# Optimization experiments

Hardware: AMD Instinct MI355X
Metric: run time of the kernel (lower is better)

The kernel has to match this reference:

```python
import jax, jax.numpy as jnp
import numpy as np
from jax import ops

NEG_SLOPE = 0.2
EPS = 1e-5


def layer_norm(v, g, b):
    mu = jnp.mean(v, axis=-1, keepdims=True)
    var = jnp.mean(jnp.square(v - mu), axis=-1, keepdims=True)
    return (v - mu) * jax.lax.rsqrt(var + EPS) * g + b


def gat_conv(x, src, dst, W, a_src, a_dst, bias, N, H, C, concat):
    # linear projection, per-head view [N, H, C]
    h = (x @ W).reshape(N, H, C)
    alpha_src = jnp.sum(h * a_src, axis=-1)  # [N, H]
    alpha_dst = jnp.sum(h * a_dst, axis=-1)  # [N, H]
    # per-edge raw attention logits [E, H]
    e = alpha_src[src] + alpha_dst[dst]
    e = jnp.where(e > 0, e, NEG_SLOPE * e)  # leaky relu
    # segment softmax over destination node
    m = ops.segment_max(e, dst, num_segments=N)  # [N, H]
    a = jnp.exp(e - m[dst])
    s = ops.segment_sum(a, dst, num_segments=N)  # [N, H]
    a = a / s[dst]
    # weighted scatter-aggregate: [E, H, C] messages -> [N, H, C]
    out = ops.segment_sum(h[src] * a[:, :, None], dst, num_segments=N)
    if concat:
        return out.reshape(N, H * C) + bias
    return jnp.mean(out, axis=1) + bias


def setup_inputs() -> dict:
    key = jax.random.key(0)
    ks = jax.random.split(key, 16)
    N, E, IN, H, C1, C2 = 50000, 800000, 128, 4, 64, 64
    sd_in = 1.0 / np.sqrt(IN)
    sd_h = 1.0 / np.sqrt(H * C1)
    return {
        "x": jax.random.normal(ks[0], (N, IN), jnp.float32),
        "edge_index": jax.random.randint(ks[1], (2, E), 0, N, jnp.int64),
        # GAT layer 1 (in -> H*C1, concat)
        "W1": jax.random.normal(ks[2], (IN, H * C1), jnp.float32) * sd_in,
        "att_src1": jax.random.normal(ks[3], (H, C1), jnp.float32) * sd_in,
        "att_dst1": jax.random.normal(ks[4], (H, C1), jnp.float32) * sd_in,
        "bias1": jnp.zeros((H * C1,), jnp.float32),
        "g1": jnp.ones((H * C1,), jnp.float32),
        "b1": jnp.zeros((H * C1,), jnp.float32),
        # GAT layer 2 (H*C1 -> C2, mean over heads)
        "W2": jax.random.normal(ks[5], (H * C1, H * C2), jnp.float32) * sd_h,
        "att_src2": jax.random.normal(ks[6], (H, C2), jnp.float32) * sd_h,
        "att_dst2": jax.random.normal(ks[7], (H, C2), jnp.float32) * sd_h,
        "bias2": jnp.zeros((C2,), jnp.float32),
        "g2": jnp.ones((C2,), jnp.float32),
        "b2": jnp.zeros((C2,), jnp.float32),
        # residual projection (in != out)
        "Wres": jax.random.normal(ks[8], (IN, C2), jnp.float32) * sd_in,
        "bres": jnp.zeros((C2,), jnp.float32),
    }


def reference(x, edge_index, W1, att_src1, att_dst1, bias1, g1, b1,
              W2, att_src2, att_dst2, bias2, g2, b2, Wres, bres):
    N = x.shape[0]
    H, C1 = att_src1.shape
    C2 = att_src2.shape[1]
    # PyG GATConv add_self_loops=True
    loop = jnp.arange(N, dtype=edge_index.dtype)
    src = jnp.concatenate([edge_index[0], loop])
    dst = jnp.concatenate([edge_index[1], loop])

    identity = x @ Wres + bres
    h1 = gat_conv(x, src, dst, W1, att_src1, att_dst1, bias1, N, H, C1, concat=True)
    h1 = jax.nn.elu(layer_norm(h1, g1, b1))  # dropout inactive (eval)
    h2 = gat_conv(h1, src, dst, W2, att_src2, att_dst2, bias2, N, H, C2, concat=False)
    h2 = layer_norm(h2, g2, b2)
    return jax.nn.elu(h2 + identity)
```

## Files before the change

### kernel.cpp

```cpp
#include <hip/hip_runtime.h>
#include <math.h>

#define HH 4
#define CC 64
#define HC 256
#define CAP 96

static constexpr float NEG_SLOPE = 0.2f;
static constexpr float LN_EPS = 1e-5f;

typedef __attribute__((ext_vector_type(8))) short short8;
typedef __attribute__((ext_vector_type(4))) float floatx4;
typedef __attribute__((ext_vector_type(4))) unsigned int uintx4;

__device__ __forceinline__ float bf2f(unsigned short u) {
  return __uint_as_float(((unsigned int)u) << 16);
}
__device__ __forceinline__ unsigned short f2bf(float f) {
  unsigned int u = __float_as_uint(f);
  u = (u + 0x7fff + ((u >> 16) & 1)) >> 16;
  return (unsigned short)u;
}
__device__ __forceinline__ unsigned int pack2bf(float a, float b) {
  return (unsigned int)f2bf(a) | ((unsigned int)f2bf(b) << 16);
}

__device__ __forceinline__ void macc8(float* acc, uintx4 h, float w) {
  acc[0] += w * __uint_as_float(h.x << 16);
  acc[1] += w * __uint_as_float(h.x & 0xffff0000u);
  acc[2] += w * __uint_as_float(h.y << 16);
  acc[3] += w * __uint_as_float(h.y & 0xffff0000u);
  acc[4] += w * __uint_as_float(h.z << 16);
  acc[5] += w * __uint_as_float(h.z & 0xffff0000u);
  acc[6] += w * __uint_as_float(h.w << 16);
  acc[7] += w * __uint_as_float(h.w & 0xffff0000u);
}

__device__ __forceinline__ short8 ldA8(const unsigned short* A, size_t idx) {
  return *(const short8*)(A + idx);
}
__device__ __forceinline__ short8 ldA8(const float* A, size_t idx) {
  const float4 u = *(const float4*)(A + idx);
  const float4 v = *(const float4*)(A + idx + 4);
  short8 r;
  r[0] = (short)f2bf(u.x); r[1] = (short)f2bf(u.y);
  r[2] = (short)f2bf(u.z); r[3] = (short)f2bf(u.w);
  r[4] = (short)f2bf(v.x); r[5] = (short)f2bf(v.y);
  r[6] = (short)f2bf(v.z); r[7] = (short)f2bf(v.w);
  return r;
}

__global__ __launch_bounds__(256) void prep_kernel(
    const float* __restrict__ W1, const float* __restrict__ W2,
    const float* __restrict__ Wres,
    unsigned short* __restrict__ wt1c, unsigned short* __restrict__ wt2,
    int* __restrict__ deg, int N) {
  const int idx = blockIdx.x * 256 + threadIdx.x;
  if (idx < 49152) {
    const int r = idx >> 7, k = idx & 127;
    float v = 0.f;
    if (r < 256) v = W1[k * 256 + r];
    else if (r < 320) v = Wres[k * 64 + (r - 256)];
    wt1c[idx] = f2bf(v);
  } else if (idx < 49152 + 65536) {
    const int i = idx - 49152;
    const int r = i >> 8, k = i & 255;
    wt2[i] = f2bf(W2[k * 256 + r]);
  } else if (idx < 49152 + 65536 + N) {
    deg[idx - 49152 - 65536] = 0;
  }
}

__global__ __launch_bounds__(256) void scatter_bump(
    const int* __restrict__ srcs, const int* __restrict__ dsts,
    int* __restrict__ deg, int* __restrict__ col, int E, int N) {
  const int e = blockIdx.x * 256 + threadIdx.x;
  if (e >= E + N) return;
  int s, d;
  if (e < E) { s = srcs[e]; d = dsts[e]; }
  else       { s = e - E; d = s; }
  const int pos = atomicAdd(&deg[d], 1);
  col[d * CAP + pos] = s;
}

template <typename AT>
__global__ __launch_bounds__(256) void gemm128(
    const AT* __restrict__ A, const unsigned short* __restrict__ BT,
    unsigned short* __restrict__ Chm,
    float* __restrict__ ident, const float* __restrict__ bres,
    const float* __restrict__ att_src, const float* __restrict__ att_dst,
    float* __restrict__ as_, float* __restrict__ ad_,
    int M, int K) {
  __shared__ unsigned short As[128][40];
  __shared__ unsigned short Bs[128][40];
  const int tid = threadIdx.x;
  const int w = tid >> 6, lane = tid & 63;
  const int q = lane >> 4, mr = lane & 15;
  const int rh = w >> 1, ch = w & 1;
  const int row0 = blockIdx.x * 128;
  const int col0 = blockIdx.y * 128;
  const int sr = tid >> 2;
  const int sk = (tid & 3) * 8;

  floatx4 acc[4][4] = {};

  short8 a0 = {}, a1 = {}, b0, b1;
  {
    const int r0 = row0 + sr, r1 = row0 + sr + 64;
    if (r0 < M) a0 = ldA8(A, (size_t)r0 * K + sk);
    if (r1 < M) a1 = ldA8(A, (size_t)r1 * K + sk);
    b0 = *(const short8*)(BT + (size_t)(col0 + sr) * K + sk);
    b1 = *(const short8*)(BT + (size_t)(col0 + sr + 64) * K + sk);
  }
  for (int k0 = 0; k0 < K; k0 += 32) {
    *(short8*)(&As[sr][sk]) = a0;
    *(short8*)(&As[sr + 64][sk]) = a1;
    *(short8*)(&Bs[sr][sk]) = b0;
    *(short8*)(&Bs[sr + 64][sk]) = b1;
    __syncthreads();
    const int kn = k0 + 32;
    if (kn < K) {
      const int r0 = row0 + sr, r1 = row0 + sr + 64;
      a0 = (r0 < M) ? ldA8(A, (size_t)r0 * K + kn + sk) : short8{};
      a1 = (r1 < M) ? ldA8(A, (size_t)r1 * K + kn + sk) : short8{};
      b0 = *(const short8*)(BT + (size_t)(col0 + sr) * K + kn + sk);
      b1 = *(const short8*)(BT + (size_t)(col0 + sr + 64) * K + kn + sk);
    }
    short8 af[4], bf[4];
#pragma unroll
    for (int i = 0; i < 4; ++i)
      af[i] = *(const short8*)(&As[rh * 64 + i * 16 + mr][q * 8]);
#pragma unroll
    for (int j = 0; j < 4; ++j)
      bf[j] = *(const short8*)(&Bs[ch * 64 + j * 16 + mr][q * 8]);
#pragma unroll
    for (int i = 0; i < 4; ++i)
#pragma unroll
      for (int j = 0; j < 4; ++j)
        acc[i][j] = __builtin_amdgcn_mfma_f32_16x16x32_bf16(af[i], bf[j], acc[i][j], 0, 0, 0);
    __syncthreads();
  }
  if (col0 < 256) {
    const int hh = (col0 >> 6) + ch;
#pragma unroll
    for (int i = 0; i < 4; ++i)
#pragma unroll
      for (int j = 0; j < 4; ++j)
#pragma unroll
        for (int rr = 0; rr < 4; ++rr) {
          const int row = row0 + rh * 64 + i * 16 + q * 4 + rr;
          if (row < M)
            Chm[((size_t)hh * M + row) * 64 + j * 16 + mr] = f2bf(acc[i][j][rr]);
        }
    float pa[16] = {}, pb[16] = {};
#pragma unroll
    for (int j = 0; j < 4; ++j) {
      const float a_s = att_src[hh * 64 + j * 16 + mr];
      const float a_d = att_dst[hh * 64 + j * 16 + mr];
#pragma unroll
      for (int i = 0; i < 4; ++i)
#pragma unroll
        for (int rr = 0; rr < 4; ++rr) {
          pa[i * 4 + rr] += acc[i][j][rr] * a_s;
          pb[i * 4 + rr] += acc[i][j][rr] * a_d;
        }
    }
#pragma unroll
    for (int off = 1; off < 16; off <<= 1) {
#pragma unroll
      for (int t = 0; t < 16; ++t) {
        pa[t] += __shfl_xor(pa[t], off);
        pb[t] += __shfl_xor(pb[t], off);
      }
    }
    if (mr == 0) {
#pragma unroll
      for (int i = 0; i < 4; ++i)
#pragma unroll
        for (int rr = 0; rr < 4; ++rr) {
          const int row = row0 + rh * 64 + i * 16 + q * 4 + rr;
          if (row < M) {
            as_[row * 4 + hh] = pa[i * 4 + rr];
            ad_[row * 4 + hh] = pb[i * 4 + rr];
          }
        }
    }
  } else if (ch == 0) {
#pragma unroll
    for (int i = 0; i < 4; ++i)
#pragma unroll
      for (int j = 0; j < 4; ++j)
#pragma unroll
        for (int rr = 0; rr < 4; ++rr) {
          const int row = row0 + rh * 64 + i * 16 + q * 4 + rr;
          if (row < M) {
            const int cc = j * 16 + mr;
            ident[(size_t)row * 64 + cc] = acc[i][j][rr] + bres[cc];
          }
        }
  }
}

__global__ __launch_bounds__(256) void agg_gather(
    const int* __restrict__ deg, const int* __restrict__ col,
    const float* __restrict__ as_, const float* __restrict__ ad_,
    const unsigned short* __restrict__ hlin_hm,
    unsigned short* __restrict__ agg, int N) {
  const int b = blockIdx.x;
  const int hh = b & 3;
  const int w = threadIdx.x >> 6, lane = threadIdx.x & 63;
  const int g = lane >> 4;
  const int sub = (lane >> 3) & 1;
  const int cg = lane & 7;
  const int el = lane & 15;
  const int gb = lane & 48;
  const int n = (b >> 3) * 32 + ((b >> 2) & 1) * 16 + w * 4 + g;
  const bool valid = n < N;
  const int n_c = valid ? n : 0;
  const uintx4* hb = (const uintx4*)(hlin_hm + (size_t)hh * N * 64) + cg;
  const float adv = ad_[n_c * 4 + hh];
  const int cnt = valid ? deg[n_c] : 0;
  const int* cbase = col + n_c * CAP;
  float acc[8] = {};
  float wsum = 0.f;
  for (int off = 0;; off += 16) {
    const int len = cnt - off;
    int lm = len > 16 ? 16 : (len < 0 ? 0 : len);
    lm = max(lm, __shfl_xor(lm, 16));
    lm = max(lm, __shfl_xor(lm, 32));
    if (lm == 0) break;
    int s_l = 0;
    float w_l = 0.f;
    if (el < len) {
      s_l = cbase[off + el];
      float v = as_[s_l * 4 + hh] + adv;
      v = v > 0.f ? v : NEG_SLOPE * v;
      w_l = __expf(v);
    }
    wsum += w_l;
    int j = 0;
    for (; j + 4 <= lm; j += 4) {
      const int sA = __shfl(s_l, gb + j + sub);
      const int sB = __shfl(s_l, gb + j + 2 + sub);
      const float wA = __shfl(w_l, gb + j + sub);
      const float wB = __shfl(w_l, gb + j + 2 + sub);
      const uintx4 hA = hb[(size_t)sA * 8];
      const uintx4 hB = hb[(size_t)sB * 8];
      macc8(acc, hA, wA);
      macc8(acc, hB, wB);
    }
    for (; j < lm; j += 2) {
      const int s = __shfl(s_l, gb + j + sub);
      const float wt = __shfl(w_l, gb + j + sub);
      macc8(acc, hb[(size_t)s * 8], wt);
    }
  }
  wsum += __shfl_xor(wsum, 1);
  wsum += __shfl_xor(wsum, 2);
  wsum += __shfl_xor(wsum, 4);
  wsum += __shfl_xor(wsum, 8);
#pragma unroll
  for (int t = 0; t < 8; ++t) acc[t] += __shfl_xor(acc[t], 8);
  if (sub == 0 && valid) {
    const float inv = 1.0f / wsum;
    uintx4 o;
    o.x = pack2bf(acc[0] * inv, acc[1] * inv);
    o.y = pack2bf(acc[2] * inv, acc[3] * inv);
    o.z = pack2bf(acc[4] * inv, acc[5] * inv);
    o.w = pack2bf(acc[6] * inv, acc[7] * inv);
    ((uintx4*)(agg + ((size_t)hh * N + n) * 64))[cg] = o;
  }
}

__global__ __launch_bounds__(256) void combine_ln1(
    const unsigned short* __restrict__ agg, const float* __restrict__ bias1,
    const float* __restrict__ g1, const float* __restrict__ b1,
    unsigned short* __restrict__ h1, int N) {
  const int n = blockIdx.x;
  const int tid = threadIdx.x;
  const int hh = tid >> 6, lane = tid & 63;
  const float val = bf2f(agg[((size_t)hh * N + n) * 64 + lane]) + bias1[tid];
  float s1 = val, s2 = val * val;
#pragma unroll
  for (int off = 32; off > 0; off >>= 1) {
    s1 += __shfl_down(s1, off);
    s2 += __shfl_down(s2, off);
  }
  __shared__ float ws1[4], ws2[4];
  if (lane == 0) { ws1[hh] = s1; ws2[hh] = s2; }
  __syncthreads();
  const float tot1 = ws1[0] + ws1[1] + ws1[2] + ws1[3];
  const float tot2 = ws2[0] + ws2[1] + ws2[2] + ws2[3];
  const float mu = tot1 * (1.0f / HC);
  const float var = tot2 * (1.0f / HC) - mu * mu;
  float y = (val - mu) * rsqrtf(var + LN_EPS) * g1[tid] + b1[tid];
  y = y > 0.f ? y : expm1f(y);
  h1[(size_t)n * HC + tid] = f2bf(y);
}

__global__ __launch_bounds__(256) void combine_final(
    const unsigned short* __restrict__ agg, const float* __restrict__ ident,
    const float* __restrict__ bias2, const float* __restrict__ g2,
    const float* __restrict__ b2, float* __restrict__ out, int N) {
  const int n = blockIdx.x * 4 + (threadIdx.x >> 6);
  const int c = threadIdx.x & 63;
  if (n >= N) return;
  float v = 0.25f * (bf2f(agg[((size_t)0 * N + n) * 64 + c]) +
                     bf2f(agg[((size_t)1 * N + n) * 64 + c]) +
                     bf2f(agg[((size_t)2 * N + n) * 64 + c]) +
                     bf2f(agg[((size_t)3 * N + n) * 64 + c])) +
            bias2[c];
  float s1 = v, s2 = v * v;
#pragma unroll
  for (int off = 32; off > 0; off >>= 1) {
    s1 += __shfl_down(s1, off);
    s2 += __shfl_down(s2, off);
  }
  s1 = __shfl(s1, 0);
  s2 = __shfl(s2, 0);
  const float mu = s1 * (1.0f / 64.0f);
  const float var = s2 * (1.0f / 64.0f) - mu * mu;
  float y = (v - mu) * rsqrtf(var + LN_EPS) * g2[c] + b2[c];
  y += ident[(size_t)n * 64 + c];
  out[(size_t)n * 64 + c] = y > 0.f ? y : expm1f(y);
}

extern "C" void kernel_launch(void* const* d_in, const int* in_sizes, int n_in,
                              void* d_out, int out_size, void* d_ws, size_t ws_size,
                              hipStream_t stream) {
  const float* x        = (const float*)d_in[0];
  const int*   ei       = (const int*)d_in[1];
  const float* W1       = (const float*)d_in[2];
  const float* att_src1 = (const float*)d_in[3];
  const float* att_dst1 = (const float*)d_in[4];
  const float* bias1    = (const float*)d_in[5];
  const float* g1       = (const float*)d_in[6];
  const float* b1       = (const float*)d_in[7];
  const float* W2       = (const float*)d_in[8];
  const float* att_src2 = (const float*)d_in[9];
  const float* att_dst2 = (const float*)d_in[10];
  const float* bias2    = (const float*)d_in[11];
  const float* g2       = (const float*)d_in[12];
  const float* b2       = (const float*)d_in[13];
  const float* Wres     = (const float*)d_in[14];
  const float* bres     = (const float*)d_in[15];

  const int N = in_sizes[0] / 128;
  const int E = in_sizes[1] / 2;
  const int IN = 128;

  const int* srcs = ei;
  const int* dsts = ei + E;

  char* p = (char*)d_ws;
  auto alloc = [&](size_t bytes) {
    char* r = p;
    p += (bytes + 255) & ~(size_t)255;
    return r;
  };
  float* ident  = (float*)alloc((size_t)N * 64 * 4);
  float* as_    = (float*)alloc((size_t)N * HH * 4);
  float* ad_    = (float*)alloc((size_t)N * HH * 4);
  int* deg      = (int*)alloc((size_t)N * 4);
  int* col      = (int*)alloc((size_t)N * CAP * 4);
  unsigned short* hlin_hm = (unsigned short*)alloc((size_t)N * HC * 2);
  unsigned short* h1b     = (unsigned short*)alloc((size_t)N * HC * 2);
  unsigned short* aggb    = (unsigned short*)alloc((size_t)4 * N * 64 * 2);
  unsigned short* wt1c = (unsigned short*)alloc((size_t)384 * IN * 2);
  unsigned short* wt2  = (unsigned short*)alloc((size_t)HC * HC * 2);

  const int m128 = (N + 127) / 128;
  const int prep_items = 49152 + 65536 + N;
  const int gatherblocks = ((N + 31) / 32) * 8;
  dim3 blk(256);

  prep_kernel<<<(prep_items + 255) / 256, blk, 0, stream>>>(
      W1, W2, Wres, wt1c, wt2, deg, N);

  scatter_bump<<<(E + N + 255) / 256, blk, 0, stream>>>(srcs, dsts, deg, col, E, N);

  gemm128<float><<<dim3(m128, 3), blk, 0, stream>>>(
      x, wt1c, hlin_hm, ident, bres, att_src1, att_dst1, as_, ad_, N, IN);
  agg_gather<<<gatherblocks, blk, 0, stream>>>(deg, col, as_, ad_, hlin_hm, aggb, N);
  combine_ln1<<<N, blk, 0, stream>>>(aggb, bias1, g1, b1, h1b, N);

  gemm128<unsigned short><<<dim3(m128, 2), blk, 0, stream>>>(
      h1b, wt2, hlin_hm, nullptr, nullptr, att_src2, att_dst2, as_, ad_, N, HC);
  agg_gather<<<gatherblocks, blk, 0, stream>>>(deg, col, as_, ad_, hlin_hm, aggb, N);
  combine_final<<<(N + 3) / 4, blk, 0, stream>>>(aggb, ident, bias2, g2, b2,
                                                 (float*)d_out, N);
}
```

Before: 367.4 us.

## Fuse edge scatter into first GEMM launch as interleaved extra blocks

Removes the standalone scatter_bump kernel and folds its work into the layer-1 GEMM grid. Every third block (up to S of them) handles 2048 edges of atomic CSR bucket fill, and the remaining blocks run the GEMM tile indexed through a flattened 1D grid. This saves a kernel launch and lets the memory-bound atomic scatter overlap the compute-bound GEMM. In exchange each GEMM block does extra index arithmetic, and scatter blocks waste the shared memory that is declared for the GEMM tiles.

After: 335.4 us. 1.1x faster.

```diff
diff --git a/kernel.cpp b/kernel.cpp
--- a/kernel.cpp
+++ b/kernel.cpp
@@ -71,18 +71,6 @@
   }
 }
 
-__global__ __launch_bounds__(256) void scatter_bump(
-    const int* __restrict__ srcs, const int* __restrict__ dsts,
-    int* __restrict__ deg, int* __restrict__ col, int E, int N) {
-  const int e = blockIdx.x * 256 + threadIdx.x;
-  if (e >= E + N) return;
-  int s, d;
-  if (e < E) { s = srcs[e]; d = dsts[e]; }
-  else       { s = e - E; d = s; }
-  const int pos = atomicAdd(&deg[d], 1);
-  col[d * CAP + pos] = s;
-}
-
 template <typename AT>
 __global__ __launch_bounds__(256) void gemm128(
     const AT* __restrict__ A, const unsigned short* __restrict__ BT,
@@ -90,15 +78,41 @@
     float* __restrict__ ident, const float* __restrict__ bres,
     const float* __restrict__ att_src, const float* __restrict__ att_dst,
     float* __restrict__ as_, float* __restrict__ ad_,
-    int M, int K) {
+    int M, int K, int GM,
+    const int* __restrict__ srcs, const int* __restrict__ dsts,
+    int* __restrict__ deg, int* __restrict__ col, int E, int N, int S) {
+  const int bid = blockIdx.x;
+  const int tid = threadIdx.x;
+  int gid = bid;
+  if (S > 0) {
+    const int q = bid / 3;
+    const bool is_scatter = (bid % 3 == 2) && (q < S);
+    if (is_scatter) {
+      const int base = q * 2048 + tid * 8;
+#pragma unroll
+      for (int k = 0; k < 8; ++k) {
+        const int e = base + k;
+        if (e < E + N) {
+          int s, d;
+          if (e < E) { s = srcs[e]; d = dsts[e]; }
+          else       { s = e - E; d = s; }
+          const int pos = atomicAdd(&deg[d], 1);
+          col[d * CAP + pos] = s;
+        }
+      }
+      return;
+    }
+    gid = bid - (q < S ? q : S);
+  }
+  const int bx = gid % GM, by = gid / GM;
+
   __shared__ unsigned short As[128][40];
   __shared__ unsigned short Bs[128][40];
-  const int tid = threadIdx.x;
   const int w = tid >> 6, lane = tid & 63;
-  const int q = lane >> 4, mr = lane & 15;
+  const int q4 = lane >> 4, mr = lane & 15;
   const int rh = w >> 1, ch = w & 1;
-  const int row0 = blockIdx.x * 128;
-  const int col0 = blockIdx.y * 128;
+  const int row0 = bx * 128;
+  const int col0 = by * 128;
   const int sr = tid >> 2;
   const int sk = (tid & 3) * 8;
 
@@ -129,10 +143,10 @@
     short8 af[4], bf[4];
 #pragma unroll
     for (int i = 0; i < 4; ++i)
-      af[i] = *(const short8*)(&As[rh * 64 + i * 16 + mr][q * 8]);
+      af[i] = *(const short8*)(&As[rh * 64 + i * 16 + mr][q4 * 8]);
 #pragma unroll
     for (int j = 0; j < 4; ++j)
-      bf[j] = *(const short8*)(&Bs[ch * 64 + j * 16 + mr][q * 8]);
+      bf[j] = *(const short8*)(&Bs[ch * 64 + j * 16 + mr][q4 * 8]);
 #pragma unroll
     for (int i = 0; i < 4; ++i)
 #pragma unroll
@@ -148,7 +162,7 @@
       for (int j = 0; j < 4; ++j)
 #pragma unroll
         for (int rr = 0; rr < 4; ++rr) {
-          const int row = row0 + rh * 64 + i * 16 + q * 4 + rr;
+          const int row = row0 + rh * 64 + i * 16 + q4 * 4 + rr;
           if (row < M)
             Chm[((size_t)hh * M + row) * 64 + j * 16 + mr] = f2bf(acc[i][j][rr]);
         }
@@ -178,7 +192,7 @@
       for (int i = 0; i < 4; ++i)
 #pragma unroll
         for (int rr = 0; rr < 4; ++rr) {
-          const int row = row0 + rh * 64 + i * 16 + q * 4 + rr;
+          const int row = row0 + rh * 64 + i * 16 + q4 * 4 + rr;
           if (row < M) {
             as_[row * 4 + hh] = pa[i * 4 + rr];
             ad_[row * 4 + hh] = pb[i * 4 + rr];
@@ -192,7 +206,7 @@
       for (int j = 0; j < 4; ++j)
 #pragma unroll
         for (int rr = 0; rr < 4; ++rr) {
-          const int row = row0 + rh * 64 + i * 16 + q * 4 + rr;
+          const int row = row0 + rh * 64 + i * 16 + q4 * 4 + rr;
           if (row < M) {
             const int cc = j * 16 + mr;
             ident[(size_t)row * 64 + cc] = acc[i][j][rr] + bres[cc];
@@ -372,20 +386,22 @@
   const int m128 = (N + 127) / 128;
   const int prep_items = 49152 + 65536 + N;
   const int gatherblocks = ((N + 31) / 32) * 8;
+  const int G1 = m128 * 3;
+  const int S  = (E + N + 2047) / 2048;
   dim3 blk(256);
 
   prep_kernel<<<(prep_items + 255) / 256, blk, 0, stream>>>(
       W1, W2, Wres, wt1c, wt2, deg, N);
 
-  scatter_bump<<<(E + N + 255) / 256, blk, 0, stream>>>(srcs, dsts, deg, col, E, N);
-
-  gemm128<float><<<dim3(m128, 3), blk, 0, stream>>>(
-      x, wt1c, hlin_hm, ident, bres, att_src1, att_dst1, as_, ad_, N, IN);
+  gemm128<float><<<G1 + S, blk, 0, stream>>>(
+      x, wt1c, hlin_hm, ident, bres, att_src1, att_dst1, as_, ad_, N, IN, m128,
+      srcs, dsts, deg, col, E, N, S);
   agg_gather<<<gatherblocks, blk, 0, stream>>>(deg, col, as_, ad_, hlin_hm, aggb, N);
   combine_ln1<<<N, blk, 0, stream>>>(aggb, bias1, g1, b1, h1b, N);
 
-  gemm128<unsigned short><<<dim3(m128, 2), blk, 0, stream>>>(
-      h1b, wt2, hlin_hm, nullptr, nullptr, att_src2, att_dst2, as_, ad_, N, HC);
+  gemm128<unsigned short><<<m128 * 2, blk, 0, stream>>>(
+      h1b, wt2, hlin_hm, nullptr, nullptr, att_src2, att_dst2, as_, ad_, N, HC, m128,
+      nullptr, nullptr, nullptr, nullptr, 0, N, 0);
   agg_gather<<<gatherblocks, blk, 0, stream>>>(deg, col, as_, ad_, hlin_hm, aggb, N);
   combine_final<<<(N + 3) / 4, blk, 0, stream>>>(aggb, ident, bias2, g2, b2,
                                                  (float*)d_out, N);
```
